# Kernel tuning notes

Hardware: AMD Instinct MI355X
Metric: run time of the kernel (lower is better)

## Reference

```python
import jax, jax.numpy as jnp
import numpy as np
import math

B, S, D, H, R = 4, 2048, 512, 8, 8  # R = k+1 relative slots per direction


def setup_inputs() -> dict:
    key = jax.random.key(0)
    ks = jax.random.split(key, 16)
    dk = D // H
    sc = 1.0 / math.sqrt(D)
    return {
        "query": jax.random.normal(ks[0], (B, S, D), jnp.float32),
        "key": jax.random.normal(ks[1], (B, S, D), jnp.float32),
        "value": jax.random.normal(ks[2], (B, S, D), jnp.float32),
        "start_nodes": jax.random.randint(ks[3], (B, H, R, S), 0, S, jnp.int64 if jax.config.jax_enable_x64 else jnp.int32),
        "end_nodes": jax.random.randint(ks[4], (B, H, R, S), 0, S, jnp.int64 if jax.config.jax_enable_x64 else jnp.int32),
        "rel_q": jax.random.normal(ks[5], (1, H, 2 * R, dk), jnp.float32),
        "rel_k": jax.random.normal(ks[6], (1, H, 2 * R, dk), jnp.float32),
        "rel_v": jax.random.normal(ks[7], (1, H, 2 * R, dk), jnp.float32),
        "Wq": jax.random.normal(ks[8], (D, D), jnp.float32) * sc,
        "bq": jnp.zeros((D,), jnp.float32),
        "Wk": jax.random.normal(ks[9], (D, D), jnp.float32) * sc,
        "bk": jnp.zeros((D,), jnp.float32),
        "Wv": jax.random.normal(ks[10], (D, D), jnp.float32) * sc,
        "bv": jnp.zeros((D,), jnp.float32),
        "Wo": jax.random.normal(ks[11], (D, D), jnp.float32) * sc,
        "bo": jnp.zeros((D,), jnp.float32),
    }


def reference(query, key, value, start_nodes, end_nodes, rel_q, rel_k, rel_v,
              Wq, bq, Wk, bk, Wv, bv, Wo, bo):
    Bs, Ss, Ds = query.shape
    Hs = start_nodes.shape[1]
    dk = Ds // Hs

    def proj(x, W, b):
        return (x @ W.T + b).reshape(Bs, Ss, Hs, dk).transpose(0, 2, 1, 3)  # [B,H,S,dk]

    q = proj(query, Wq, bq)
    k = proj(key, Wk, bk)
    v = proj(value, Wv, bv)

    start_mask = start_nodes == -1
    sn = jnp.where(start_mask, 0, start_nodes)  # -1 padding -> 0 (masked out below)
    qidx = jnp.concatenate([end_nodes, sn], axis=2)  # [B,H,2R,S]
    kidx = jnp.concatenate([sn, end_nodes], axis=2)

    bi = jnp.arange(Bs)[:, None, None, None]
    hi = jnp.arange(Hs)[None, :, None, None]
    q_ctx = q[bi, hi, qidx]  # [B,H,2R,S,dk]
    k_ctx = k[bi, hi, kidx]
    v_ctx = v[bi, hi, kidx]

    # c2c + c2p + p2c, scale_factor = 3 (rel_q and rel_k both provided)
    scores = ((q_ctx * k_ctx).sum(-1)
              + (q_ctx * rel_k[:, :, :, None, :]).sum(-1)
              + (rel_q[:, :, :, None, :] * k_ctx).sum(-1))
    scores = scores / (3.0 * jnp.sqrt(jnp.asarray(dk, scores.dtype)))

    # mask: padded edges masked in both halves; first S flat entries always masked
    mask = jnp.concatenate([start_mask, start_mask], axis=2).reshape(Bs, Hs, -1)
    mask = mask.at[:, :, :Ss].set(True)
    sflat = jnp.exp(jnp.where(mask, -1e9, scores.reshape(Bs, Hs, -1)))  # [B,H,2R*S]

    qf = qidx.reshape(Bs, Hs, -1)
    b2 = jnp.arange(Bs)[:, None, None]
    h2 = jnp.arange(Hs)[None, :, None]
    # scatter-add softmax denominator over destination nodes, then gather back
    denom = jnp.zeros((Bs, Hs, Ss), sflat.dtype).at[b2, h2, qf].add(sflat)
    denom = jnp.where(denom == 0, -1e9, denom)
    probs = (sflat / denom[b2, h2, qf]).reshape(Bs, Hs, -1, Ss, 1)  # [B,H,2R,S,1]

    attn_v = probs * (v_ctx + rel_v[:, :, :, None, :])  # [B,H,2R,S,dk]
    out = jnp.zeros((Bs, Hs, Ss, dk), attn_v.dtype).at[b2, h2, qf].add(
        attn_v.reshape(Bs, Hs, -1, dk))  # scatter-add aggregation over edges

    out = out.transpose(0, 2, 1, 3).reshape(Bs, Ss, Ds)
    return out @ Wo.T + bo
```

## Files before the change

### kernel.cpp

```cpp
#include <hip/hip_runtime.h>
#include <math.h>

#define B_ 4
#define S_ 2048
#define D_ 512
#define H_ 8
#define R_ 8
#define DK_ 64
#define NEDGE (B_*H_*2*R_*S_)
#define ELLCAP 64

typedef __attribute__((ext_vector_type(8))) short bf16x8;
typedef __attribute__((ext_vector_type(8))) unsigned short ushort8_t;
typedef __attribute__((ext_vector_type(4))) float f32x4;

#define AS1q const __attribute__((address_space(1)))
#define AS3q __attribute__((address_space(3)))

__device__ inline unsigned short f2bf(float f) {
    unsigned u = __builtin_bit_cast(unsigned, f);
    u += 0x7fffu + ((u >> 16) & 1u);
    return (unsigned short)(u >> 16);
}
__device__ inline float bf2f(unsigned short u) {
    return __builtin_bit_cast(float, ((unsigned)u) << 16);
}

__global__ __launch_bounds__(256) void prep(
    const float* __restrict__ query, const float* __restrict__ key,
    const float* __restrict__ value,
    const float* __restrict__ Wq, const float* __restrict__ Wk,
    const float* __restrict__ Wv, const float* __restrict__ Wo,
    unsigned short* __restrict__ qc, unsigned short* __restrict__ kc,
    unsigned short* __restrict__ vc,
    unsigned short* __restrict__ wqb, unsigned short* __restrict__ wkb,
    unsigned short* __restrict__ wvb, unsigned short* __restrict__ wob,
    int* __restrict__ deg)
{
    int bid = blockIdx.x;
    if (bid < 12288) {
        int z = bid >> 12;
        const float* x = (z == 0) ? query : (z == 1) ? key : value;
        unsigned short* y = (z == 0) ? qc : (z == 1) ? kc : vc;
        size_t i = ((size_t)(bid & 4095) * 256 + threadIdx.x) * 4;
        float4 v = *(const float4*)&x[i];
        *(ushort4*)&y[i] = make_ushort4(f2bf(v.x), f2bf(v.y), f2bf(v.z), f2bf(v.w));
    } else if (bid < 13312) {
        int r = bid - 12288;
        int z = r >> 8;
        const float* x = (z == 0) ? Wq : (z == 1) ? Wk : (z == 2) ? Wv : Wo;
        unsigned short* y = (z == 0) ? wqb : (z == 1) ? wkb : (z == 2) ? wvb : wob;
        size_t i = ((size_t)(r & 255) * 256 + threadIdx.x) * 4;
        float4 v = *(const float4*)&x[i];
        *(ushort4*)&y[i] = make_ushort4(f2bf(v.x), f2bf(v.y), f2bf(v.z), f2bf(v.w));
    } else {
        int r = bid - 13312;
        *(int4*)&deg[((size_t)r * 256 + threadIdx.x) * 4] = make_int4(0, 0, 0, 0);
    }
}

template<int TN>
__global__ __launch_bounds__(256) void gemm_bf16(
    const unsigned short* __restrict__ A0, const unsigned short* __restrict__ A1,
    const unsigned short* __restrict__ A2,
    const unsigned short* __restrict__ W0, const unsigned short* __restrict__ W1,
    const unsigned short* __restrict__ W2,
    const float* __restrict__ bi0, const float* __restrict__ bi1, const float* __restrict__ bi2,
    unsigned short* __restrict__ C0, unsigned short* __restrict__ C1,
    unsigned short* __restrict__ C2,
    float* __restrict__ Cf, int a_bhsd)
{
    constexpr int NFR = TN / 32;
    __shared__ unsigned short As[128 * 64];
    __shared__ unsigned short Bs[TN * 64];
    const int z = blockIdx.z;
    const unsigned short* A = (z == 0) ? A0 : (z == 1) ? A1 : A2;
    const unsigned short* W = (z == 0) ? W0 : (z == 1) ? W1 : W2;
    const float* bias        = (z == 0) ? bi0 : (z == 1) ? bi1 : bi2;
    unsigned short* C        = (z == 0) ? C0 : (z == 1) ? C1 : C2;

    const int t    = threadIdx.x;
    const int lane = t & 63;
    const int w    = t >> 6;
    const int wm   = w >> 1, wn = w & 1;
    const int m0   = blockIdx.x * 128;
    const int n0   = blockIdx.y * TN;

    const int lr    = lane >> 3;
    const int cglob = (lane & 7) ^ lr;

    f32x4 acc[4][NFR] = {};

    for (int kk = 0; kk < D_; kk += 64) {
        #pragma unroll
        for (int i = 0; i < 4; ++i) {
            int rowl = w * 32 + i * 8;
            int m = m0 + rowl + lr;
            const unsigned short* ga;
            if (a_bhsd) {
                int b = m >> 11, s = m & (S_ - 1), h = kk >> 6;
                ga = A + ((((size_t)b * H_ + h) * S_ + s) << 6) + cglob * 8;
            } else {
                ga = A + (size_t)m * D_ + kk + cglob * 8;
            }
            __builtin_amdgcn_global_load_lds((AS1q unsigned*)ga,
                (AS3q unsigned*)(As + rowl * 64), 16, 0, 0);
        }
        #pragma unroll
        for (int i = 0; i < TN / 32; ++i) {
            int rowl = w * (TN / 4) + i * 8;
            const unsigned short* gb =
                W + (size_t)(n0 + rowl + lr) * D_ + kk + cglob * 8;
            __builtin_amdgcn_global_load_lds((AS1q unsigned*)gb,
                (AS3q unsigned*)(Bs + rowl * 64), 16, 0, 0);
        }
        __syncthreads();

        #pragma unroll
        for (int ks = 0; ks < 64; ks += 32) {
            const int c0 = ks >> 3;
            bf16x8 af[4], bfr[NFR];
            #pragma unroll
            for (int mi = 0; mi < 4; ++mi) {
                int row = wm * 64 + mi * 16 + (lane & 15);
                int cp  = (c0 + (lane >> 4)) ^ (lane & 7);
                af[mi] = *(const bf16x8*)&As[row * 64 + cp * 8];
            }
            #pragma unroll
            for (int nj = 0; nj < NFR; ++nj) {
                int row = wn * (TN / 2) + nj * 16 + (lane & 15);
                int cp  = (c0 + (lane >> 4)) ^ (lane & 7);
                bfr[nj] = *(const bf16x8*)&Bs[row * 64 + cp * 8];
            }
            #pragma unroll
            for (int mi = 0; mi < 4; ++mi)
                #pragma unroll
                for (int nj = 0; nj < NFR; ++nj)
                    acc[mi][nj] = __builtin_amdgcn_mfma_f32_16x16x32_bf16(af[mi], bfr[nj], acc[mi][nj], 0, 0, 0);
        }
        __syncthreads();
    }

    #pragma unroll
    for (int mi = 0; mi < 4; ++mi) {
        #pragma unroll
        for (int nj = 0; nj < NFR; ++nj) {
            #pragma unroll
            for (int r = 0; r < 4; ++r) {
                int m = m0 + wm * 64 + mi * 16 + (lane >> 4) * 4 + r;
                int n = n0 + wn * (TN / 2) + nj * 16 + (lane & 15);
                float val = acc[mi][nj][r] + bias[n];
                if (Cf) {
                    Cf[(size_t)m * D_ + n] = val;
                } else {
                    int b = m >> 11, s = m & (S_ - 1);
                    int h = n >> 6,  d = n & 63;
                    C[((((size_t)b * H_ + h) * S_ + s) << 6) + d] = f2bf(val);
                }
            }
        }
    }
}

__global__ __launch_bounds__(256) void fill_ell(
    const int* __restrict__ start_nodes, const int* __restrict__ end_nodes,
    int* __restrict__ deg, unsigned short* __restrict__ ell)
{
    int f = blockIdx.x * 256 + threadIdx.x;
    int s    = f & (S_ - 1);
    int rest = f >> 11;
    int r2   = rest & 15;
    int bh   = rest >> 4;
    if (r2 == 0) return;
    int r  = r2 & 7;
    int idx = (bh * R_ + r) * S_ + s;
    int sn = start_nodes[idx];
    if (sn == -1) return;
    int en = end_nodes[idx];
    int dst = (r2 < R_) ? en : sn;
    int ki  = (r2 < R_) ? sn : en;
    int g = bh * S_ + dst;
    int pos = atomicAdd(&deg[g], 1);
    if (pos < ELLCAP)
        ell[(size_t)g * ELLCAP + pos] = (unsigned short)((r2 << 11) | ki);
}

__global__ __launch_bounds__(256) void edge_gather(
    const unsigned short* __restrict__ q, const unsigned short* __restrict__ k_,
    const unsigned short* __restrict__ v_,
    const float* __restrict__ rel_q, const float* __restrict__ rel_k,
    const float* __restrict__ rel_v,
    const int* __restrict__ deg, const unsigned short* __restrict__ ell,
    unsigned short* __restrict__ attn)
{
    int raw = blockIdx.x;
    int xcd = raw & 7;
    int loc = raw >> 3;
    int bh  = xcd * 4 + (loc >> 9);
    int wid = threadIdx.x >> 6;
    int dst = (loc & 511) * 4 + wid;
    int lane = threadIdx.x & 63;
    int grp = lane >> 3;
    int sub = lane & 7;
    int h = bh & 7;
    int g = bh * S_ + dst;
    size_t node_base = ((size_t)bh << 11);

    ushort8_t q8 = *(const ushort8_t*)&q[((node_base + dst) << 6) + sub * 8];
    float qv[8];
    #pragma unroll
    for (int i = 0; i < 8; ++i) qv[i] = bf2f(q8[i]);

    int n = deg[g];
    if (n > ELLCAP) n = ELLCAP;
    int d_all = (int)ell[(size_t)g * ELLCAP + lane];

    float den = 0.f;
    float o[8] = {};
    #pragma unroll 2
    for (int j = 0; j < n; j += 8) {
        int slot = j + grp;
        int d = __shfl(d_all, slot);
        bool valid = slot < n;
        int ki = d & (S_ - 1);
        int r2 = (d >> 11) & 15;
        size_t koff = ((node_base + ki) << 6) + sub * 8;
        int roff = (((h << 4) + r2) << 6) + sub * 8;
        ushort8_t k8 = *(const ushort8_t*)&k_[koff];
        float rkv[8], rqv[8], rvv[8];
        *(float4*)&rkv[0] = *(const float4*)&rel_k[roff];
        *(float4*)&rkv[4] = *(const float4*)&rel_k[roff + 4];
        *(float4*)&rqv[0] = *(const float4*)&rel_q[roff];
        *(float4*)&rqv[4] = *(const float4*)&rel_q[roff + 4];
        float p = 0.f;
        #pragma unroll
        for (int i = 0; i < 8; ++i)
            p = fmaf(bf2f(k8[i]), qv[i] + rqv[i], fmaf(qv[i], rkv[i], p));
        p += __shfl_xor(p, 1);
        p += __shfl_xor(p, 2);
        p += __shfl_xor(p, 4);
        float sf = valid ? __expf(p * (1.0f / 24.0f)) : 0.f;
        ushort8_t v8 = *(const ushort8_t*)&v_[koff];
        *(float4*)&rvv[0] = *(const float4*)&rel_v[roff];
        *(float4*)&rvv[4] = *(const float4*)&rel_v[roff + 4];
        den += sf;
        #pragma unroll
        for (int i = 0; i < 8; ++i)
            o[i] = fmaf(sf, bf2f(v8[i]) + rvv[i], o[i]);
    }
    den += __shfl_xor(den, 8); den += __shfl_xor(den, 16); den += __shfl_xor(den, 32);
    #pragma unroll
    for (int i = 0; i < 8; ++i) {
        o[i] += __shfl_xor(o[i], 8);
        o[i] += __shfl_xor(o[i], 16);
        o[i] += __shfl_xor(o[i], 32);
    }
    if (grp == 0) {
        float inv = (den > 0.f) ? 1.0f / den : 0.f;
        ushort8_t r;
        #pragma unroll
        for (int i = 0; i < 8; ++i) r[i] = f2bf(o[i] * inv);
        *(ushort8_t*)&attn[((node_base + dst) << 6) + sub * 8] = r;
    }
}

extern "C" void kernel_launch(void* const* d_in, const int* in_sizes, int n_in,
                              void* d_out, int out_size, void* d_ws, size_t ws_size,
                              hipStream_t stream) {
    const float* query = (const float*)d_in[0];
    const float* key   = (const float*)d_in[1];
    const float* value = (const float*)d_in[2];
    const int* start_nodes = (const int*)d_in[3];
    const int* end_nodes   = (const int*)d_in[4];
    const float* rel_q = (const float*)d_in[5];
    const float* rel_k = (const float*)d_in[6];
    const float* rel_v = (const float*)d_in[7];
    const float* Wq = (const float*)d_in[8];
    const float* bq = (const float*)d_in[9];
    const float* Wk = (const float*)d_in[10];
    const float* bk = (const float*)d_in[11];
    const float* Wv = (const float*)d_in[12];
    const float* bv = (const float*)d_in[13];
    const float* Wo = (const float*)d_in[14];
    const float* bo = (const float*)d_in[15];
    float* out = (float*)d_out;

    const size_t NQ = (size_t)B_ * H_ * S_ * DK_;
    const size_t NW = (size_t)D_ * D_;
    const size_t NG = (size_t)B_ * H_ * S_;
    unsigned short* p = (unsigned short*)d_ws;
    unsigned short* qc = p;            p += NQ;
    unsigned short* kc = p;            p += NQ;
    unsigned short* vc = p;            p += NQ;
    unsigned short* q  = p;            p += NQ;
    unsigned short* k  = p;            p += NQ;
    unsigned short* v  = p;            p += NQ;
    unsigned short* attn = p;          p += NQ;
    unsigned short* wqb = p;           p += NW;
    unsigned short* wkb = p;           p += NW;
    unsigned short* wvb = p;           p += NW;
    unsigned short* wob = p;           p += NW;
    unsigned short* ell = p;           p += NG * ELLCAP;
    int* deg = (int*)p;

    prep<<<13376, 256, 0, stream>>>(query, key, value, Wq, Wk, Wv, Wo,
                                    qc, kc, vc, wqb, wkb, wvb, wob, deg);

    fill_ell<<<NEDGE / 256, 256, 0, stream>>>(start_nodes, end_nodes, deg, ell);

    dim3 ggrid(B_ * S_ / 128, D_ / 128, 3);
    gemm_bf16<128><<<ggrid, 256, 0, stream>>>(qc, kc, vc, wqb, wkb, wvb, bq, bk, bv,
                                              q, k, v, nullptr, 0);

    edge_gather<<<(B_ * H_ * S_) / 4, 256, 0, stream>>>(
        q, k, v, rel_q, rel_k, rel_v, deg, ell, attn);

    dim3 ogrid(B_ * S_ / 128, D_ / 64, 1);
    gemm_bf16<64><<<ogrid, 256, 0, stream>>>(attn, attn, attn, wob, wob, wob, bo, bo, bo,
                                             nullptr, nullptr, nullptr, out, 1);
}
```

Baseline: 247.7 us.

## Build ELL lists with shared-memory counters and store rel tables as bf16

The global-atomic ELL fill becomes a per-(batch, head, 256-node range) block. Each block scans every edge of its batch-head and counts degrees with shared-memory atomics, so the separate deg zeroing in prep goes away. The relative position tables are also converted to bf16 in prep, halving their load width in edge_gather. The trade-off is that each edge is now read 8 times across range blocks, and the rel tables lose precision.

```diff
diff --git a/kernel.cpp b/kernel.cpp
--- a/kernel.cpp
+++ b/kernel.cpp
@@ -8,6 +8,7 @@
 #define R_ 8
 #define DK_ 64
 #define NEDGE (B_*H_*2*R_*S_)
+#define EPB   (2*R_*S_)
 #define ELLCAP 64
 
 typedef __attribute__((ext_vector_type(8))) short bf16x8;
@@ -31,32 +32,39 @@
     const float* __restrict__ value,
     const float* __restrict__ Wq, const float* __restrict__ Wk,
     const float* __restrict__ Wv, const float* __restrict__ Wo,
+    const float* __restrict__ rel_q, const float* __restrict__ rel_k,
+    const float* __restrict__ rel_v,
     unsigned short* __restrict__ qc, unsigned short* __restrict__ kc,
     unsigned short* __restrict__ vc,
     unsigned short* __restrict__ wqb, unsigned short* __restrict__ wkb,
     unsigned short* __restrict__ wvb, unsigned short* __restrict__ wob,
-    int* __restrict__ deg)
+    unsigned short* __restrict__ rqb, unsigned short* __restrict__ rkb,
+    unsigned short* __restrict__ rvb)
 {
     int bid = blockIdx.x;
+    const float* x;
+    unsigned short* y;
+    size_t i;
     if (bid < 12288) {
         int z = bid >> 12;
-        const float* x = (z == 0) ? query : (z == 1) ? key : value;
-        unsigned short* y = (z == 0) ? qc : (z == 1) ? kc : vc;
-        size_t i = ((size_t)(bid & 4095) * 256 + threadIdx.x) * 4;
-        float4 v = *(const float4*)&x[i];
-        *(ushort4*)&y[i] = make_ushort4(f2bf(v.x), f2bf(v.y), f2bf(v.z), f2bf(v.w));
+        x = (z == 0) ? query : (z == 1) ? key : value;
+        y = (z == 0) ? qc : (z == 1) ? kc : vc;
+        i = ((size_t)(bid & 4095) * 256 + threadIdx.x) * 4;
     } else if (bid < 13312) {
         int r = bid - 12288;
         int z = r >> 8;
-        const float* x = (z == 0) ? Wq : (z == 1) ? Wk : (z == 2) ? Wv : Wo;
-        unsigned short* y = (z == 0) ? wqb : (z == 1) ? wkb : (z == 2) ? wvb : wob;
-        size_t i = ((size_t)(r & 255) * 256 + threadIdx.x) * 4;
-        float4 v = *(const float4*)&x[i];
-        *(ushort4*)&y[i] = make_ushort4(f2bf(v.x), f2bf(v.y), f2bf(v.z), f2bf(v.w));
+        x = (z == 0) ? Wq : (z == 1) ? Wk : (z == 2) ? Wv : Wo;
+        y = (z == 0) ? wqb : (z == 1) ? wkb : (z == 2) ? wvb : wob;
+        i = ((size_t)(r & 255) * 256 + threadIdx.x) * 4;
     } else {
         int r = bid - 13312;
-        *(int4*)&deg[((size_t)r * 256 + threadIdx.x) * 4] = make_int4(0, 0, 0, 0);
-    }
+        int z = r >> 3;
+        x = (z == 0) ? rel_q : (z == 1) ? rel_k : rel_v;
+        y = (z == 0) ? rqb : (z == 1) ? rkb : rvb;
+        i = ((size_t)(r & 7) * 256 + threadIdx.x) * 4;
+    }
+    float4 v = *(const float4*)&x[i];
+    *(ushort4*)&y[i] = make_ushort4(f2bf(v.x), f2bf(v.y), f2bf(v.z), f2bf(v.w));
 }
 
 template<int TN>
@@ -162,34 +170,47 @@
     }
 }
 
-__global__ __launch_bounds__(256) void fill_ell(
+__global__ __launch_bounds__(1024) void build_ell(
     const int* __restrict__ start_nodes, const int* __restrict__ end_nodes,
     int* __restrict__ deg, unsigned short* __restrict__ ell)
 {
-    int f = blockIdx.x * 256 + threadIdx.x;
-    int s    = f & (S_ - 1);
-    int rest = f >> 11;
-    int r2   = rest & 15;
-    int bh   = rest >> 4;
-    if (r2 == 0) return;
-    int r  = r2 & 7;
-    int idx = (bh * R_ + r) * S_ + s;
-    int sn = start_nodes[idx];
-    if (sn == -1) return;
-    int en = end_nodes[idx];
-    int dst = (r2 < R_) ? en : sn;
-    int ki  = (r2 < R_) ? sn : en;
-    int g = bh * S_ + dst;
-    int pos = atomicAdd(&deg[g], 1);
-    if (pos < ELLCAP)
-        ell[(size_t)g * ELLCAP + pos] = (unsigned short)((r2 << 11) | ki);
+    __shared__ int cnt[256];
+    const int bh  = blockIdx.x >> 3;
+    const int oct = blockIdx.x & 7;
+    const int t   = threadIdx.x;
+    const int dlo = oct << 8;
+    if (t < 256) cnt[t] = 0;
+    __syncthreads();
+
+    const int base_idx = bh * (R_ * S_);
+    for (int f = t; f < EPB; f += 1024) {
+        int r2 = f >> 11;
+        if (r2 == 0) continue;
+        int s = f & (S_ - 1);
+        int r = r2 & 7;
+        int idx = base_idx + r * S_ + s;
+        int sn = start_nodes[idx];
+        if (sn == -1) continue;
+        int en = end_nodes[idx];
+        int dst = (r2 < R_) ? en : sn;
+        unsigned rel = (unsigned)(dst - dlo);
+        if (rel < 256u) {
+            int ki = (r2 < R_) ? sn : en;
+            int pos = atomicAdd(&cnt[rel], 1);
+            if (pos < ELLCAP)
+                ell[((size_t)(bh * S_ + dst)) * ELLCAP + pos] =
+                    (unsigned short)((r2 << 11) | ki);
+        }
+    }
+    __syncthreads();
+    if (t < 256) deg[bh * S_ + dlo + t] = cnt[t];
 }
 
 __global__ __launch_bounds__(256) void edge_gather(
     const unsigned short* __restrict__ q, const unsigned short* __restrict__ k_,
     const unsigned short* __restrict__ v_,
-    const float* __restrict__ rel_q, const float* __restrict__ rel_k,
-    const float* __restrict__ rel_v,
+    const unsigned short* __restrict__ rel_q, const unsigned short* __restrict__ rel_k,
+    const unsigned short* __restrict__ rel_v,
     const int* __restrict__ deg, const unsigned short* __restrict__ ell,
     unsigned short* __restrict__ attn)
 {
@@ -224,29 +245,24 @@
         bool valid = slot < n;
         int ki = d & (S_ - 1);
         int r2 = (d >> 11) & 15;
-        size_t koff = ((node_base + ki) << 6) + sub * 8;
-        int roff = (((h << 4) + r2) << 6) + sub * 8;
-        ushort8_t k8 = *(const ushort8_t*)&k_[koff];
-        float rkv[8], rqv[8], rvv[8];
-        *(float4*)&rkv[0] = *(const float4*)&rel_k[roff];
-        *(float4*)&rkv[4] = *(const float4*)&rel_k[roff + 4];
-        *(float4*)&rqv[0] = *(const float4*)&rel_q[roff];
-        *(float4*)&rqv[4] = *(const float4*)&rel_q[roff + 4];
+        ushort8_t k8  = *(const ushort8_t*)&k_  [((node_base + ki) << 6) + sub * 8];
+        ushort8_t rk8 = *(const ushort8_t*)&rel_k[(((h << 4) + r2) << 6) + sub * 8];
+        ushort8_t rq8 = *(const ushort8_t*)&rel_q[(((h << 4) + r2) << 6) + sub * 8];
         float p = 0.f;
         #pragma unroll
         for (int i = 0; i < 8; ++i)
-            p = fmaf(bf2f(k8[i]), qv[i] + rqv[i], fmaf(qv[i], rkv[i], p));
+            p = fmaf(bf2f(k8[i]), qv[i] + bf2f(rq8[i]),
+                     fmaf(qv[i], bf2f(rk8[i]), p));
         p += __shfl_xor(p, 1);
         p += __shfl_xor(p, 2);
         p += __shfl_xor(p, 4);
         float sf = valid ? __expf(p * (1.0f / 24.0f)) : 0.f;
-        ushort8_t v8 = *(const ushort8_t*)&v_[koff];
-        *(float4*)&rvv[0] = *(const float4*)&rel_v[roff];
-        *(float4*)&rvv[4] = *(const float4*)&rel_v[roff + 4];
+        ushort8_t v8  = *(const ushort8_t*)&v_  [((node_base + ki) << 6) + sub * 8];
+        ushort8_t rv8 = *(const ushort8_t*)&rel_v[(((h << 4) + r2) << 6) + sub * 8];
         den += sf;
         #pragma unroll
         for (int i = 0; i < 8; ++i)
-            o[i] = fmaf(sf, bf2f(v8[i]) + rvv[i], o[i]);
+            o[i] = fmaf(sf, bf2f(v8[i]) + bf2f(rv8[i]), o[i]);
     }
     den += __shfl_xor(den, 8); den += __shfl_xor(den, 16); den += __shfl_xor(den, 32);
     #pragma unroll
@@ -287,6 +303,7 @@
 
     const size_t NQ = (size_t)B_ * H_ * S_ * DK_;
     const size_t NW = (size_t)D_ * D_;
+    const size_t NR = (size_t)H_ * 2 * R_ * DK_;
     const size_t NG = (size_t)B_ * H_ * S_;
     unsigned short* p = (unsigned short*)d_ws;
     unsigned short* qc = p;            p += NQ;
@@ -300,20 +317,25 @@
     unsigned short* wkb = p;           p += NW;
     unsigned short* wvb = p;           p += NW;
     unsigned short* wob = p;           p += NW;
+    unsigned short* rqb = p;           p += NR;
+    unsigned short* rkb = p;           p += NR;
+    unsigned short* rvb = p;           p += NR;
     unsigned short* ell = p;           p += NG * ELLCAP;
     int* deg = (int*)p;
 
-    prep<<<13376, 256, 0, stream>>>(query, key, value, Wq, Wk, Wv, Wo,
-                                    qc, kc, vc, wqb, wkb, wvb, wob, deg);
-
-    fill_ell<<<NEDGE / 256, 256, 0, stream>>>(start_nodes, end_nodes, deg, ell);
+    prep<<<13336, 256, 0, stream>>>(query, key, value, Wq, Wk, Wv, Wo,
+                                    rel_q, rel_k, rel_v,
+                                    qc, kc, vc, wqb, wkb, wvb, wob,
+                                    rqb, rkb, rvb);
+
+    build_ell<<<B_ * H_ * 8, 1024, 0, stream>>>(start_nodes, end_nodes, deg, ell);
 
     dim3 ggrid(B_ * S_ / 128, D_ / 128, 3);
     gemm_bf16<128><<<ggrid, 256, 0, stream>>>(qc, kc, vc, wqb, wkb, wvb, bq, bk, bv,
                                               q, k, v, nullptr, 0);
 
     edge_gather<<<(B_ * H_ * S_) / 4, 256, 0, stream>>>(
-        q, k, v, rel_q, rel_k, rel_v, deg, ell, attn);
+        q, k, v, rqb, rkb, rvb, deg, ell, attn);
 
     dim3 ogrid(B_ * S_ / 128, D_ / 64, 1);
     gemm_bf16<64><<<ogrid, 256, 0, stream>>>(attn, attn, attn, wob, wob, wob, bo, bo, bo,
```

Result: faster. 237.6 us (-4.1%).
